# Optimization experiments

Hardware: AMD Instinct MI355X
Metric: run time of the kernel (lower is better)

## Reference

```python
import jax, jax.numpy as jnp
import numpy as np

B, L, D, H, R, E = 4, 2048, 256, 4, 128, 32768
HD = D // H  # head dim of long-range attention
FF = 4 * D   # positionwise FFN hidden
NEG_SLOPE = 0.2  # GATConv leaky_relu slope


def setup_inputs() -> dict:
    key = jax.random.key(0)
    ks = jax.random.split(key, 16)
    n = lambda k, sh: jax.random.normal(k, sh, dtype=jnp.float32) * 0.05
    z = lambda sh: jnp.zeros(sh, dtype=jnp.float32)
    o = lambda sh: jnp.ones(sh, dtype=jnp.float32)
    return {
        "s": jax.random.normal(ks[0], (B, L, D), dtype=jnp.float32),
        "gat_W": n(ks[1], (D, H * D)),
        "gat_att_src": n(ks[2], (H, D)),
        "gat_att_dst": n(ks[3], (H, D)),
        "gat_b": z((H * D,)),
        "short_W": n(ks[4], (H * D, D)), "short_b": z((D,)),
        "q_W": n(ks[5], (D, D)), "q_b": z((D,)),
        "k_W": n(ks[6], (D, D)), "k_b": z((D,)),
        "v_W": n(ks[7], (D, D)), "v_b": z((D,)),
        "o_W": n(ks[8], (D, D)), "o_b": z((D,)),
        "p_W": n(ks[9], (D, R)), "p_b": z((R,)),
        "lnq_g": o((D,)), "lnq_b": z((D,)),
        "lnk_g": o((D,)), "lnk_b": z((D,)),
        "lnv_g": o((D,)), "lnv_b": z((D,)),
        "ln1_g": o((D,)), "ln1_b": z((D,)),
        "ln2_g": o((D,)), "ln2_b": z((D,)),
        "f1_W": n(ks[10], (D, FF)), "f1_b": z((FF,)),
        "f2_W": n(ks[11], (FF, D)), "f2_b": z((D,)),
        "edge_index": jax.random.randint(ks[12], (2, E), 0, L, dtype=jnp.int32),
    }


def _ln(x, g, b, eps=1e-5):
    mu = jnp.mean(x, -1, keepdims=True)
    var = jnp.mean(jnp.square(x - mu), -1, keepdims=True)
    return (x - mu) * jax.lax.rsqrt(var + eps) * g + b


def _forward(p, edge_index):
    s = p["s"]
    loop = jnp.arange(L, dtype=edge_index.dtype)  # add_self_loops=True
    src = jnp.concatenate([edge_index[0], loop])
    dst = jnp.concatenate([edge_index[1], loop])

    def gat_one(x):  # x: [L, D] -> [L, H*D]  (PyG GATConv, concat=True)
        h = (x @ p["gat_W"]).reshape(L, H, D)
        a_src = jnp.einsum("nhc,hc->nh", h, p["gat_att_src"])
        a_dst = jnp.einsum("nhc,hc->nh", h, p["gat_att_dst"])
        e = jax.nn.leaky_relu(a_src[src] + a_dst[dst], NEG_SLOPE)  # [Etot, H]
        m = jax.ops.segment_max(e, dst, num_segments=L)            # scatter softmax
        ex = jnp.exp(e - m[dst])
        den = jax.ops.segment_sum(ex, dst, num_segments=L)
        alpha = ex / den[dst]
        out = jax.ops.segment_sum(h[src] * alpha[:, :, None], dst, num_segments=L)
        return out.reshape(L, H * D) + p["gat_b"]

    short = jax.vmap(gat_one)(s) @ p["short_W"] + p["short_b"]  # [B,L,D]

    # DynamicLongRange (Linformer-style dynamic projection)
    q = _ln(s @ p["q_W"] + p["q_b"], p["lnq_g"], p["lnq_b"])
    k = _ln(s @ p["k_W"] + p["k_b"], p["lnk_g"], p["lnk_b"])
    v = _ln(s @ p["v_W"] + p["v_b"], p["lnv_g"], p["lnv_b"])
    pm = jax.nn.softmax(k @ p["p_W"] + p["p_b"], axis=1)          # [B,L,R], softmax over seq
    k_c = jnp.einsum("blr,bld->brd", pm, k).reshape(B, R, H, HD)
    v_c = jnp.einsum("blr,bld->brd", pm, v).reshape(B, R, H, HD)
    q_h = q.reshape(B, L, H, HD)
    scores = jnp.einsum("blhd,brhd->bhlr", q_h, k_c) / jnp.sqrt(jnp.float32(HD))
    probs = jax.nn.softmax(scores, axis=-1)
    lng = jnp.einsum("bhlr,brhd->blhd", probs, v_c).reshape(B, L, D)
    lng = lng @ p["o_W"] + p["o_b"]

    # fuse short + long, residual + LN, then positionwise FFN + residual + LN
    h1 = _ln(s + short + lng, p["ln1_g"], p["ln1_b"])
    ff = jax.nn.relu(h1 @ p["f1_W"] + p["f1_b"]) @ p["f2_W"] + p["f2_b"]
    return _ln(h1 + ff, p["ln2_g"], p["ln2_b"])


def reference(s, gat_W, gat_att_src, gat_att_dst, gat_b, short_W, short_b,
              q_W, q_b, k_W, k_b, v_W, v_b, o_W, o_b, p_W, p_b,
              lnq_g, lnq_b, lnk_g, lnk_b, lnv_g, lnv_b,
              ln1_g, ln1_b, ln2_g, ln2_b, f1_W, f1_b, f2_W, f2_b, edge_index):
    p = dict(s=s, gat_W=gat_W, gat_att_src=gat_att_src, gat_att_dst=gat_att_dst,
             gat_b=gat_b, short_W=short_W, short_b=short_b, q_W=q_W, q_b=q_b,
             k_W=k_W, k_b=k_b, v_W=v_W, v_b=v_b, o_W=o_W, o_b=o_b, p_W=p_W,
             p_b=p_b, lnq_g=lnq_g, lnq_b=lnq_b, lnk_g=lnk_g, lnk_b=lnk_b,
             lnv_g=lnv_g, lnv_b=lnv_b, ln1_g=ln1_g, ln1_b=ln1_b, ln2_g=ln2_g,
             ln2_b=ln2_b, f1_W=f1_W, f1_b=f1_b, f2_W=f2_W, f2_b=f2_b)
    return _forward(p, edge_index)
```

## Files before the change

### kernel.cpp

```cpp
#include <hip/hip_runtime.h>
#include <math.h>

#define BB   4
#define LSEQ 2048
#define DV   256
#define HH   4
#define RR   128
#define EE   32768
#define ETOT (EE + LSEQ)
#define FFD  1024

typedef unsigned short u16;
typedef __attribute__((ext_vector_type(8))) short bf16x8;
typedef __attribute__((ext_vector_type(4))) float f32x4;

__device__ __forceinline__ u16 f2bf(float f) {
    union { float f; unsigned u; } x; x.f = f;
    unsigned r = x.u + 0x7fff + ((x.u >> 16) & 1);
    return (u16)(r >> 16);
}
__device__ __forceinline__ float bf2f(u16 u) {
    union { unsigned u; float f; } x; x.u = ((unsigned)u) << 16;
    return x.f;
}

__device__ __forceinline__ void gload16(const void* g, void* l) {
    __builtin_amdgcn_global_load_lds(
        (const __attribute__((address_space(1))) unsigned int*)g,
        (__attribute__((address_space(3))) unsigned int*)l, 16, 0, 0);
}

template<int BM, int BN, int OUTBF16, int ACT>
__global__ __launch_bounds__(256) void mfma_gemm_k(
    const u16* __restrict__ A, const u16* __restrict__ BT,
    const float* __restrict__ bias, void* __restrict__ Cv,
    int M, int N, int K, int lda, int ldb, int ldc,
    long bsA1, long bsA2, long bsB1, long bsB2, long bsC1, long bsC2,
    int subH, long pairB, long pairC, int ksl, int split, float alpha)
{
    constexpr int BK = 64;
    __shared__ u16 As[BM * BK];
    __shared__ u16 Bs[BN * BK];

    int z = blockIdx.z;
    int zb = z / subH, zh = z - zb * subH;
    int mtiles = M / BM;
    int pair = blockIdx.y / mtiles;
    int mt   = blockIdx.y - pair * mtiles;

    const u16* Ab = A  + zb * bsA1 + zh * bsA2;
    const u16* Bb = BT + zb * bsB1 + zh * bsB2 + (long)pair * pairB;
    int kstart = split ? zh * ksl : 0;
    int kcount = split ? ksl : K;
    int m0 = mt * BM, n0 = blockIdx.x * BN;

    int tid  = threadIdx.x;
    int wave = tid >> 6, lane = tid & 63;
    constexpr int WGN = (BN == 128) ? 2 : 1;
    constexpr int WGM = 4 / WGN;
    constexpr int MI  = BM / (WGM * 16);
    constexpr int NI  = BN / (WGN * 16);
    int wm = wave / WGN, wn = wave - wm * WGN;
    int wmo = wm * (MI * 16);
    int wno = wn * (NI * 16);

    f32x4 acc[MI][NI];
#pragma unroll
    for (int mi = 0; mi < MI; ++mi)
#pragma unroll
        for (int ni = 0; ni < NI; ++ni)
            acc[mi][ni] = (f32x4){0.f, 0.f, 0.f, 0.f};

    constexpr int AIT = (BM * BK / 8) / 256;
    constexpr int BIT = (BN * BK / 8) / 256;

    for (int k0 = 0; k0 < kcount; k0 += BK) {
        int kb = kstart + k0;
#pragma unroll
        for (int i = 0; i < AIT; ++i) {
            int p   = i * 256 + tid;
            int row = p >> 3;
            int kc  = (p & 7) ^ (row & 7);
            const u16* gp = Ab + (long)(m0 + row) * lda + kb + kc * 8;
            gload16(gp, (char*)As + (size_t)(i * 256 + wave * 64) * 16);
        }
#pragma unroll
        for (int i = 0; i < BIT; ++i) {
            int p   = i * 256 + tid;
            int row = p >> 3;
            int kc  = (p & 7) ^ (row & 7);
            const u16* gp = Bb + (long)(n0 + row) * ldb + kb + kc * 8;
            gload16(gp, (char*)Bs + (size_t)(i * 256 + wave * 64) * 16);
        }
        asm volatile("s_waitcnt vmcnt(0)");
        __syncthreads();

        const char* Ac = (const char*)As;
        const char* Bc = (const char*)Bs;
#pragma unroll
        for (int kh = 0; kh < 2; ++kh) {
            bf16x8 af[MI], bfr[NI];
            int kby = kh * 64 + ((lane >> 4) << 4);
#pragma unroll
            for (int mi = 0; mi < MI; ++mi) {
                int r = wmo + mi * 16 + (lane & 15);
                af[mi] = *(const bf16x8*)(Ac + r * 128 + (kby ^ ((r & 7) << 4)));
            }
#pragma unroll
            for (int ni = 0; ni < NI; ++ni) {
                int r = wno + ni * 16 + (lane & 15);
                bfr[ni] = *(const bf16x8*)(Bc + r * 128 + (kby ^ ((r & 7) << 4)));
            }
#pragma unroll
            for (int mi = 0; mi < MI; ++mi)
#pragma unroll
                for (int ni = 0; ni < NI; ++ni)
                    acc[mi][ni] = __builtin_amdgcn_mfma_f32_16x16x32_bf16(
                        af[mi], bfr[ni], acc[mi][ni], 0, 0, 0);
        }
        __syncthreads();
    }

    long cb = zb * bsC1 + zh * bsC2 + (long)pair * pairC;
#pragma unroll
    for (int mi = 0; mi < MI; ++mi) {
#pragma unroll
        for (int ni = 0; ni < NI; ++ni) {
            int col = n0 + wno + ni * 16 + (lane & 15);
            float bv = bias ? bias[col] : 0.f;
#pragma unroll
            for (int j = 0; j < 4; ++j) {
                int row = m0 + wmo + mi * 16 + ((lane >> 4) << 2) + j;
                float v = acc[mi][ni][j] * alpha + bv;
                if (ACT) v = fmaxf(v, 0.f);
                long idx = (long)row * ldc + col + cb;
                if (OUTBF16) ((u16*)Cv)[idx] = f2bf(v);
                else         ((float*)Cv)[idx] = v;
            }
        }
    }
}

template<int MODE, int BM>
__global__ __launch_bounds__(256) void gemm_ln_k(
    const u16* __restrict__ A, const u16* __restrict__ BT,
    const float* __restrict__ bias, int K, int lda,
    const float* __restrict__ lg0, const float* __restrict__ lb0,
    const float* __restrict__ lg1, const float* __restrict__ lb1,
    const float* __restrict__ lg2, const float* __restrict__ lb2,
    const u16* __restrict__ resB0, const u16* __restrict__ resB1,
    u16* __restrict__ outRM, u16* __restrict__ outRM2,
    u16* __restrict__ outT, float* __restrict__ outF)
{
    constexpr int BK = 64;
    constexpr int MI = BM / 16;
    constexpr int ABYTES = BM * 128;
    __shared__ char smem[ABYTES + 32768];
    __shared__ float redS[BM][4], redQ[BM][4];
    u16* Asm = (u16*)smem;
    u16* Bsm = (u16*)(smem + ABYTES);

    int seg = blockIdx.x;
    int m0 = blockIdx.y * BM;
    int n0 = seg * 256;
    int tid = threadIdx.x, wave = tid >> 6, lane = tid & 63;
    int c = lane & 15, g = lane >> 4;

    f32x4 acc[MI][4];
#pragma unroll
    for (int mi = 0; mi < MI; ++mi)
#pragma unroll
        for (int ni = 0; ni < 4; ++ni)
            acc[mi][ni] = (f32x4){0.f, 0.f, 0.f, 0.f};

    constexpr int AIT = (BM * BK / 8) / 256;

    for (int k0 = 0; k0 < K; k0 += BK) {
#pragma unroll
        for (int i = 0; i < AIT; ++i) {
            int p   = i * 256 + tid;
            int row = p >> 3;
            int kc  = (p & 7) ^ (row & 7);
            gload16(A + (long)(m0 + row) * lda + k0 + kc * 8,
                    smem + (size_t)(i * 256 + wave * 64) * 16);
        }
#pragma unroll
        for (int i = 0; i < 8; ++i) {
            int p   = i * 256 + tid;
            int row = p >> 3;
            int kc  = (p & 7) ^ (row & 7);
            gload16(BT + (long)(n0 + row) * K + k0 + kc * 8,
                    smem + ABYTES + (size_t)(i * 256 + wave * 64) * 16);
        }
        asm volatile("s_waitcnt vmcnt(0)");
        __syncthreads();

        const char* Ac = (const char*)Asm;
        const char* Bc = (const char*)Bsm;
#pragma unroll
        for (int kh = 0; kh < 2; ++kh) {
            bf16x8 af[MI], bfr[4];
            int kby = kh * 64 + (g << 4);
#pragma unroll
            for (int mi = 0; mi < MI; ++mi) {
                int r = mi * 16 + c;
                af[mi] = *(const bf16x8*)(Ac + r * 128 + (kby ^ ((r & 7) << 4)));
            }
#pragma unroll
            for (int ni = 0; ni < 4; ++ni) {
                int r = wave * 64 + ni * 16 + c;
                bfr[ni] = *(const bf16x8*)(Bc + r * 128 + (kby ^ ((r & 7) << 4)));
            }
#pragma unroll
            for (int mi = 0; mi < MI; ++mi)
#pragma unroll
                for (int ni = 0; ni < 4; ++ni)
                    acc[mi][ni] = __builtin_amdgcn_mfma_f32_16x16x32_bf16(
                        af[mi], bfr[ni], acc[mi][ni], 0, 0, 0);
        }
        __syncthreads();
    }

#pragma unroll
    for (int mi = 0; mi < MI; ++mi)
#pragma unroll
        for (int ni = 0; ni < 4; ++ni) {
            int colL = wave * 64 + ni * 16 + c;
            float bv = bias[n0 + colL];
#pragma unroll
            for (int j = 0; j < 4; ++j) {
                int row = mi * 16 + g * 4 + j;
                float v = acc[mi][ni][j] + bv;
                if (MODE == 1) {
                    long idx = (long)(m0 + row) * 256 + colL;
                    v += bf2f(resB0[idx]) + bf2f(resB1[idx]);
                }
                if (MODE == 2) {
                    long idx = (long)(m0 + row) * 256 + colL;
                    v += bf2f(resB0[idx]);
                }
                acc[mi][ni][j] = v;
            }
        }

#pragma unroll
    for (int mi = 0; mi < MI; ++mi)
#pragma unroll
        for (int j = 0; j < 4; ++j) {
            float s1 = 0.f, q1 = 0.f;
#pragma unroll
            for (int ni = 0; ni < 4; ++ni) {
                float v = acc[mi][ni][j];
                s1 += v; q1 += v * v;
            }
#pragma unroll
            for (int m = 1; m <= 8; m <<= 1) {
                s1 += __shfl_xor(s1, m);
                q1 += __shfl_xor(q1, m);
            }
            if (c == 0) {
                int row = mi * 16 + g * 4 + j;
                redS[row][wave] = s1;
                redQ[row][wave] = q1;
            }
        }
    __syncthreads();

    const float* gam;
    const float* bet;
    if (MODE == 0) {
        gam = (seg == 0) ? lg0 : (seg == 1) ? lg1 : lg2;
        bet = (seg == 0) ? lb0 : (seg == 1) ? lb1 : lb2;
    } else { gam = lg0; bet = lb0; }

    u16* T = (u16*)smem;

    float gv[4], bv2[4];
#pragma unroll
    for (int ni = 0; ni < 4; ++ni) {
        int colL = wave * 64 + ni * 16 + c;
        gv[ni] = gam[colL];
        bv2[ni] = bet[colL];
    }

#pragma unroll
    for (int mi = 0; mi < MI; ++mi)
#pragma unroll
        for (int j = 0; j < 4; ++j) {
            int row = mi * 16 + g * 4 + j;
            float S = redS[row][0] + redS[row][1] + redS[row][2] + redS[row][3];
            float Q = redQ[row][0] + redQ[row][1] + redQ[row][2] + redQ[row][3];
            float mu = S * (1.0f / 256.f);
            float var = Q * (1.0f / 256.f) - mu * mu;
            float rs = rsqrtf(var + 1e-5f);
#pragma unroll
            for (int ni = 0; ni < 4; ++ni) {
                int colL = wave * 64 + ni * 16 + c;
                float o = (acc[mi][ni][j] - mu) * rs * gv[ni] + bv2[ni];
                long idx = (long)(m0 + row) * 256 + colL;
                if (MODE == 0) {
                    u16 ob = f2bf(o);
                    if (seg == 0)      outRM[idx]  = ob;
                    else if (seg == 1) { outRM2[idx] = ob; T[colL * 65 + row] = ob; }
                    else               T[colL * 65 + row] = ob;
                } else if (MODE == 1) {
                    outRM[idx] = f2bf(o);
                } else {
                    outF[idx] = o;
                }
            }
        }

    if (MODE == 0 && seg >= 1) {
        __syncthreads();
        int b = m0 >> 11;
        int l0 = m0 & 2047;
        u16* dst = outT + ((seg == 2) ? 2097152 : 0)
                 + (long)b * 524288 + (long)tid * 2048 + l0;
        const u16* src = T + tid * 65;
#pragma unroll
        for (int i = 0; i < 8; ++i) {
            u16 tmp[8];
#pragma unroll
            for (int k2 = 0; k2 < 8; ++k2) tmp[k2] = src[i * 8 + k2];
            *(uint4*)(dst + i * 8) = *(uint4*)tmp;
        }
    }
}

__global__ __launch_bounds__(256) void attn_k(
    const u16* __restrict__ qb, const u16* __restrict__ kcb,
    const u16* __restrict__ vcT, u16* __restrict__ lngb)
{
    __shared__ u16 Ps[64 * 128];

    int bh = blockIdx.y;
    int b = bh >> 2, h = bh & 3;
    int l0 = blockIdx.x * 64;
    int tid = threadIdx.x, wave = tid >> 6, lane = tid & 63;
    int c = lane & 15, g = lane >> 4;

    const u16* kc = kcb + (long)b * (RR * DV) + h * 64;
    const u16* qg = qb + ((long)(b * LSEQ + l0)) * DV + h * 64;
    const u16* vg = vcT + ((long)b * DV + h * 64) * RR;

    f32x4 acc[8];
#pragma unroll
    for (int mi = 0; mi < 8; ++mi) acc[mi] = (f32x4){0.f, 0.f, 0.f, 0.f};

#pragma unroll
    for (int kh = 0; kh < 2; ++kh) {
        bf16x8 bq = *(const bf16x8*)(qg + (long)(wave * 16 + c) * DV + kh * 32 + g * 8);
#pragma unroll
        for (int mi = 0; mi < 8; ++mi) {
            bf16x8 af = *(const bf16x8*)(kc + (long)(mi * 16 + c) * DV + kh * 32 + g * 8);
            acc[mi] = __builtin_amdgcn_mfma_f32_16x16x32_bf16(af, bq, acc[mi], 0, 0, 0);
        }
    }

    float mx = -INFINITY;
#pragma unroll
    for (int mi = 0; mi < 8; ++mi)
#pragma unroll
        for (int j = 0; j < 4; ++j) {
            acc[mi][j] *= 0.125f;
            mx = fmaxf(mx, acc[mi][j]);
        }
    mx = fmaxf(mx, __shfl_xor(mx, 16));
    mx = fmaxf(mx, __shfl_xor(mx, 32));
    float den = 0.f;
#pragma unroll
    for (int mi = 0; mi < 8; ++mi)
#pragma unroll
        for (int j = 0; j < 4; ++j) {
            acc[mi][j] = __expf(acc[mi][j] - mx);
            den += acc[mi][j];
        }
    den += __shfl_xor(den, 16);
    den += __shfl_xor(den, 32);
    float inv = 1.0f / den;

    int l = wave * 16 + c;
#pragma unroll
    for (int mi = 0; mi < 8; ++mi) {
        short4 sv;
        sv.x = (short)f2bf(acc[mi][0] * inv);
        sv.y = (short)f2bf(acc[mi][1] * inv);
        sv.z = (short)f2bf(acc[mi][2] * inv);
        sv.w = (short)f2bf(acc[mi][3] * inv);
        int byte = l * 256 + ((mi * 32 + g * 8) ^ ((l & 7) << 4));
        *(short4*)((char*)Ps + byte) = sv;
    }
    __syncthreads();

    f32x4 a2[4];
#pragma unroll
    for (int ni = 0; ni < 4; ++ni) a2[ni] = (f32x4){0.f, 0.f, 0.f, 0.f};
#pragma unroll
    for (int kb = 0; kb < 4; ++kb) {
        int kby = kb * 64 + (g << 4);
        bf16x8 pa = *(const bf16x8*)((char*)Ps + l * 256 + (kby ^ ((l & 7) << 4)));
#pragma unroll
        for (int ni = 0; ni < 4; ++ni) {
            bf16x8 vf = *(const bf16x8*)(vg + (long)(ni * 16 + c) * RR + kb * 32 + g * 8);
            a2[ni] = __builtin_amdgcn_mfma_f32_16x16x32_bf16(pa, vf, a2[ni], 0, 0, 0);
        }
    }
#pragma unroll
    for (int ni = 0; ni < 4; ++ni)
#pragma unroll
        for (int j = 0; j < 4; ++j) {
            int lr = wave * 16 + g * 4 + j;
            int dh = ni * 16 + c;
            lngb[((long)(b * LSEQ + l0 + lr)) * DV + h * 64 + dh] = f2bf(a2[ni][j]);
        }
}

struct WTD { const float* src; u16* dst; int K, N, toff; };
struct WTA { WTD d[9]; };

__global__ __launch_bounds__(256) void prep_k(WTA a,
    const float* __restrict__ sin, u16* __restrict__ sout,
    const float* qb_, const float* kb_, const float* vb_,
    float* qkvb, int* icnt)
{
    int bid = blockIdx.x;
    if (bid < 1312) {
        int di = 0;
#pragma unroll
        for (int i = 1; i < 9; ++i) if (bid >= a.d[i].toff) di = i;
        const float* src = a.d[di].src;
        u16* dst = a.d[di].dst;
        int K = a.d[di].K, N = a.d[di].N;
        int tix = bid - a.d[di].toff;
        int nx = N >> 5;
        int tn = tix % nx, tk = tix / nx;
        int n0 = tn * 32, k0 = tk * 32;

        __shared__ float t[32][33];
        int tx = threadIdx.x & 31, ty = threadIdx.x >> 5;
#pragma unroll
        for (int i = 0; i < 32; i += 8)
            t[ty + i][tx] = src[(long)(k0 + ty + i) * N + n0 + tx];
        __syncthreads();
#pragma unroll
        for (int i = 0; i < 32; i += 8)
            dst[(long)(n0 + ty + i) * K + k0 + tx] = f2bf(t[tx][ty + i]);
    } else if (bid < 3360) {
        int i = ((bid - 1312) * 256 + threadIdx.x) * 4;
        float4 v = *(const float4*)(sin + i);
        sout[i]     = f2bf(v.x);
        sout[i + 1] = f2bf(v.y);
        sout[i + 2] = f2bf(v.z);
        sout[i + 3] = f2bf(v.w);
    } else if (bid == 3360) {
        int i = threadIdx.x;
#pragma unroll
        for (int rep = 0; rep < 3; ++rep) {
            int j = i + rep * 256;
            qkvb[j] = (j < 256) ? qb_[j] : ((j < 512) ? kb_[j - 256] : vb_[j - 512]);
        }
    } else {
        int t = (bid - 3361) * 256 + threadIdx.x;
        if (t < 512) ((int4*)icnt)[t] = (int4){0, 0, 0, 0};
    }
}

__global__ __launch_bounds__(256) void gat_att_k(
    const u16* __restrict__ h, const float* __restrict__ att_src,
    const float* __restrict__ att_dst, float* __restrict__ a_src,
    float* __restrict__ a_dst)
{
    int row  = blockIdx.x * 4 + (threadIdx.x >> 6);
    int lane = threadIdx.x & 63;
    int c0   = lane * 16;
    int head = lane >> 4;

    float as[16], ad[16];
#pragma unroll
    for (int i = 0; i < 16; ++i) { as[i] = att_src[c0 + i]; ad[i] = att_dst[c0 + i]; }

    const u16* hr = h + (long)row * (HH * DV) + c0;
    bf16x8 v0 = *(const bf16x8*)(hr);
    bf16x8 v1 = *(const bf16x8*)(hr + 8);
    float ps = 0.f, pd = 0.f;
#pragma unroll
    for (int i = 0; i < 8; ++i) {
        float f0 = bf2f((u16)v0[i]), f1 = bf2f((u16)v1[i]);
        ps += f0 * as[i] + f1 * as[i + 8];
        pd += f0 * ad[i] + f1 * ad[i + 8];
    }
#pragma unroll
    for (int m = 1; m <= 8; m <<= 1) {
        ps += __shfl_xor(ps, m);
        pd += __shfl_xor(pd, m);
    }
    if ((lane & 15) == 0) {
        a_src[(long)row * HH + head] = ps;
        a_dst[(long)row * HH + head] = pd;
    }
}

__global__ void csr_count_k(const int* __restrict__ ei, int* __restrict__ cnt)
{
    int i = blockIdx.x * blockDim.x + threadIdx.x;
    if (i >= ETOT) return;
    int dst = (i < EE) ? ei[EE + i] : (i - EE);
    atomicAdd(&cnt[dst], 1);
}

__global__ __launch_bounds__(256) void csr_scan_k(const int* __restrict__ cnt, int* __restrict__ off)
{
    __shared__ int chunk[256];
    int tid = threadIdx.x;
    int base = tid * 8;
    int loc[8];
    int s = 0;
#pragma unroll
    for (int i = 0; i < 8; ++i) { loc[i] = s; s += cnt[base + i]; }
    chunk[tid] = s;
    __syncthreads();
    for (int st = 1; st < 256; st <<= 1) {
        int v = (tid >= st) ? chunk[tid - st] : 0;
        __syncthreads();
        chunk[tid] += v;
        __syncthreads();
    }
    int pre = (tid == 0) ? 0 : chunk[tid - 1];
#pragma unroll
    for (int i = 0; i < 8; ++i) off[base + i] = pre + loc[i];
    if (tid == 255) off[LSEQ] = chunk[255];
}

__global__ void csr_fill_k(const int* __restrict__ ei, const int* __restrict__ off,
                           int* __restrict__ cnt, int* __restrict__ bucket)
{
    int i = blockIdx.x * blockDim.x + threadIdx.x;
    if (i >= ETOT) return;
    int dst = (i < EE) ? ei[EE + i] : (i - EE);
    int p = atomicSub(&cnt[dst], 1) - 1;
    bucket[off[dst] + p] = i;
}

__global__ __launch_bounds__(256) void gat_gather_k(
    const u16* __restrict__ h, const int* __restrict__ ei,
    const int* __restrict__ off, const int* __restrict__ bucket,
    const float* __restrict__ a_src, const float* __restrict__ a_dst,
    const float* __restrict__ gat_b, u16* __restrict__ out)
{
    int wv = threadIdx.x >> 6, lane = threadIdx.x & 63;
    int id = blockIdx.x;
    int jg = id >> 3, r8 = id & 7;
    int b  = r8 >> 1;
    int n  = (jg * 2 + (r8 & 1)) * 4 + wv;
    int beg = off[n], deg = off[n + 1] - beg;

    __shared__ int   src_sh[4][64];
    __shared__ float ex_sh[4][64][4];

    const float* asrc_b = a_src + (long)b * LSEQ * HH;
    const float4 ad4 = *(const float4*)(a_dst + ((long)b * LSEQ + n) * HH);
    float adst[4] = { ad4.x, ad4.y, ad4.z, ad4.w };

    int hd = lane >> 4;
    const u16* hb = h + (long)b * LSEQ * (HH * DV) + lane * 16;
    float acc[16];
#pragma unroll
    for (int i = 0; i < 16; ++i) acc[i] = 0.f;
    float sm[4] = { 0.f, 0.f, 0.f, 0.f };

    for (int c0 = 0; c0 < deg; c0 += 64) {
        int idx = c0 + lane;
        if (idx < deg) {
            int eid = bucket[beg + idx];
            int src = (eid < EE) ? ei[eid] : (eid - EE);
            src_sh[wv][lane] = src;
            float4 as4 = *(const float4*)(asrc_b + (long)src * HH);
            float as[4] = { as4.x, as4.y, as4.z, as4.w };
#pragma unroll
            for (int hh = 0; hh < 4; ++hh) {
                float e = as[hh] + adst[hh];
                e = (e >= 0.f) ? e : 0.2f * e;
                float ex = __expf(e);
                ex_sh[wv][lane][hh] = ex;
                sm[hh] += ex;
            }
        }
        int cn = deg - c0; if (cn > 64) cn = 64;
#pragma unroll 2
        for (int j = 0; j < cn; ++j) {
            int src = src_sh[wv][j];
            float al = ex_sh[wv][j][hd];
            const u16* p = hb + (long)src * (HH * DV);
            bf16x8 v0 = *(const bf16x8*)p;
            bf16x8 v1 = *(const bf16x8*)(p + 8);
#pragma unroll
            for (int i = 0; i < 8; ++i) {
                acc[i]     += al * bf2f((u16)v0[i]);
                acc[i + 8] += al * bf2f((u16)v1[i]);
            }
        }
    }

#pragma unroll
    for (int hh = 0; hh < 4; ++hh)
#pragma unroll
        for (int m = 32; m >= 1; m >>= 1)
            sm[hh] += __shfl_xor(sm[hh], m);
    float inv = 1.0f / sm[hd];

    u16 o16[16];
    const float* gb = gat_b + lane * 16;
#pragma unroll
    for (int i = 0; i < 16; ++i) o16[i] = f2bf(acc[i] * inv + gb[i]);
    uint4* op = (uint4*)(out + ((long)b * LSEQ + n) * (HH * DV) + lane * 16);
    op[0] = ((uint4*)o16)[0];
    op[1] = ((uint4*)o16)[1];
}

__global__ __launch_bounds__(256) void colsoftmax_k(const float* __restrict__ pm,
                                                    u16* __restrict__ pmT)
{
    int r = blockIdx.x;
    int b = blockIdx.y;
    int tid = threadIdx.x, wave = tid >> 6, lane = tid & 63;
    const float* base = pm + (long)b * LSEQ * RR + r;
    u16* obase = pmT + ((long)b * RR + r) * LSEQ;

    float x[8];
#pragma unroll
    for (int i = 0; i < 8; ++i) x[i] = base[(long)(tid + i * 256) * RR];

    __shared__ float red[4];
    __shared__ float m_sh, d_sh;
    float mx = x[0];
#pragma unroll
    for (int i = 1; i < 8; ++i) mx = fmaxf(mx, x[i]);
#pragma unroll
    for (int m = 32; m >= 1; m >>= 1) mx = fmaxf(mx, __shfl_xor(mx, m));
    if (lane == 0) red[wave] = mx;
    __syncthreads();
    if (tid == 0) m_sh = fmaxf(fmaxf(red[0], red[1]), fmaxf(red[2], red[3]));
    __syncthreads();
    float m = m_sh;
    float sm = 0.f;
#pragma unroll
    for (int i = 0; i < 8; ++i) { x[i] = __expf(x[i] - m); sm += x[i]; }
#pragma unroll
    for (int mm = 32; mm >= 1; mm >>= 1) sm += __shfl_xor(sm, mm);
    if (lane == 0) red[wave] = sm;
    __syncthreads();
    if (tid == 0) d_sh = red[0] + red[1] + red[2] + red[3];
    __syncthreads();
    float inv = 1.0f / d_sh;
#pragma unroll
    for (int i = 0; i < 8; ++i) obase[tid + i * 256] = f2bf(x[i] * inv);
}

__global__ __launch_bounds__(256) void reduce_kvc_k(
    const float* __restrict__ part, u16* __restrict__ kvcb, u16* __restrict__ vcT)
{
    int pb = blockIdx.z;
    int pair = pb >> 2, b = pb & 3;
    int r0 = blockIdx.y * 32, d0 = blockIdx.x * 64;
    int tid = threadIdx.x;
    __shared__ float t[32][65];
    const float* pp = part + (long)pb * (16 * 32768);
    int r = tid >> 6;
    int d = tid & 63;
#pragma unroll
    for (int i = 0; i < 8; ++i) {
        int rr = r0 + r + i * 4;
        float s = 0.f;
#pragma unroll
        for (int sp = 0; sp < 16; ++sp)
            s += pp[(long)sp * 32768 + rr * 256 + d0 + d];
        kvcb[(long)pb * 32768 + rr * 256 + d0 + d] = f2bf(s);
        t[r + i * 4][d] = s;
    }
    if (pair == 0) return;
    __syncthreads();
    int dd = tid >> 2, rb = (tid & 3) * 8;
    u16 o8[8];
#pragma unroll
    for (int k = 0; k < 8; ++k) o8[k] = f2bf(t[rb + k][dd]);
    *(uint4*)(vcT + ((long)(b * 256 + d0 + dd)) * 128 + r0 + rb) = *(uint4*)o8;
}

extern "C" void kernel_launch(void* const* d_in, const int* in_sizes, int n_in,
                              void* d_out, int out_size, void* d_ws, size_t ws_size,
                              hipStream_t stream)
{
    const float* s        = (const float*)d_in[0];
    const float* gat_W    = (const float*)d_in[1];
    const float* att_src  = (const float*)d_in[2];
    const float* att_dst  = (const float*)d_in[3];
    const float* gat_b    = (const float*)d_in[4];
    const float* short_W  = (const float*)d_in[5];
    const float* short_b  = (const float*)d_in[6];
    const float* q_W      = (const float*)d_in[7];
    const float* q_b      = (const float*)d_in[8];
    const float* k_W      = (const float*)d_in[9];
    const float* k_b      = (const float*)d_in[10];
    const float* v_W      = (const float*)d_in[11];
    const float* v_b      = (const float*)d_in[12];
    const float* o_W      = (const float*)d_in[13];
    const float* o_b      = (const float*)d_in[14];
    const float* p_W      = (const float*)d_in[15];
    const float* p_b      = (const float*)d_in[16];
    const float* lnq_g    = (const float*)d_in[17];
    const float* lnq_b    = (const float*)d_in[18];
    const float* lnk_g    = (const float*)d_in[19];
    const float* lnk_b    = (const float*)d_in[20];
    const float* lnv_g    = (const float*)d_in[21];
    const float* lnv_b    = (const float*)d_in[22];
    const float* ln1_g    = (const float*)d_in[23];
    const float* ln1_b    = (const float*)d_in[24];
    const float* ln2_g    = (const float*)d_in[25];
    const float* ln2_b    = (const float*)d_in[26];
    const float* f1_W     = (const float*)d_in[27];
    const float* f1_b     = (const float*)d_in[28];
    const float* f2_W     = (const float*)d_in[29];
    const float* f2_b     = (const float*)d_in[30];
    const int*   ei       = (const int*)d_in[31];
    float* out = (float*)d_out;

    const size_t MB = 1024 * 1024;
    char* W = (char*)d_ws;
    u16*   sb      = (u16*)(W);
    u16*   gatT    = (u16*)(W + 4*MB);
    u16*   shortT  = (u16*)(W + 4*MB + 524288);
    u16*   qkvT    = (u16*)(W + 4*MB + 1048576);
    u16*   oT      = (u16*)(W + 4*MB + 1441792);
    u16*   pT      = (u16*)(W + 4*MB + 1572864);
    u16*   f1T     = (u16*)(W + 4*MB + 1638400);
    u16*   f2T     = (u16*)(W + 4*MB + 2162688);
    float* qkvb    = (float*)(W + 4*MB + 2686976);
    int*   ioff    = (int*)(W + 4*MB + 2690048);
    int*   icnt    = (int*)(W + 4*MB + 2699264);
    int*   ibucket = (int*)(W + 4*MB + 2707456);
    u16*   h       = (u16*)(W + 8*MB);
    u16*   ffh     = (u16*)(W + 8*MB);
    u16*   gat_out = (u16*)(W + 24*MB);
    u16*   h1b     = (u16*)(W + 40*MB);
    u16*   shortb16= (u16*)(W + 44*MB);
    float* pmraw   = (float*)(W + 48*MB);
    float* part    = (float*)(W + 48*MB);
    u16*   lngb    = (u16*)(W + 48*MB);
    u16*   qb      = (u16*)(W + 72*MB);
    u16*   kb      = (u16*)(W + 76*MB);
    u16*   kvT     = (u16*)(W + 84*MB);
    u16*   pmT     = (u16*)(W + 92*MB);
    u16*   kvcb    = (u16*)(W + 94*MB);
    u16*   vcT     = (u16*)(W + 94*MB + 524288);
    float* a_src   = (float*)(W + 95*MB);
    float* a_dst   = (float*)(W + 95*MB + 131072);

    const int ML = BB * LSEQ;

    WTA wa;
    wa.d[0] = { gat_W,   gatT,            256, 1024, 0    };
    wa.d[1] = { short_W, shortT,         1024,  256, 256  };
    wa.d[2] = { q_W,     qkvT,            256,  256, 512  };
    wa.d[3] = { k_W,     qkvT + 65536,    256,  256, 576  };
    wa.d[4] = { v_W,     qkvT + 131072,   256,  256, 640  };
    wa.d[5] = { o_W,     oT,              256,  256, 704  };
    wa.d[6] = { p_W,     pT,              256,  128, 768  };
    wa.d[7] = { f1_W,    f1T,             256, 1024, 800  };
    wa.d[8] = { f2_W,    f2T,            1024,  256, 1056 };
    prep_k<<<3363, 256, 0, stream>>>(wa, s, sb, q_b, k_b, v_b, qkvb, icnt);

    csr_count_k<<<(ETOT + 255) / 256, 256, 0, stream>>>(ei, icnt);
    csr_scan_k<<<1, 256, 0, stream>>>(icnt, ioff);
    csr_fill_k<<<(ETOT + 255) / 256, 256, 0, stream>>>(ei, ioff, icnt, ibucket);

    mfma_gemm_k<128, 128, 1, 0><<<dim3(8, 64, 1), 256, 0, stream>>>(
        sb, gatT, nullptr, h, ML, 1024, 256, 256, 256, 1024,
        0, 0, 0, 0, 0, 0, 1, 0, 0, 0, 0, 1.f);
    gat_att_k<<<ML / 4, 256, 0, stream>>>(h, att_src, att_dst, a_src, a_dst);
    gat_gather_k<<<2048, 256, 0, stream>>>(h, ei, ioff, ibucket,
                                           a_src, a_dst, gat_b, gat_out);
    mfma_gemm_k<64, 128, 1, 0><<<dim3(2, 128, 1), 256, 0, stream>>>(
        gat_out, shortT, short_b, shortb16, ML, 256, 1024, 1024, 1024, 256,
        0, 0, 0, 0, 0, 0, 1, 0, 0, 0, 0, 1.f);

    gemm_ln_k<0, 64><<<dim3(3, 128), 256, 0, stream>>>(
        sb, qkvT, qkvb, 256, 256,
        lnq_g, lnq_b, lnk_g, lnk_b, lnv_g, lnv_b,
        nullptr, nullptr, qb, kb, kvT, nullptr);

    mfma_gemm_k<64, 64, 0, 0><<<dim3(2, 128, 1), 256, 0, stream>>>(
        kb, pT, p_b, pmraw, ML, 128, 256, 256, 256, 128,
        0, 0, 0, 0, 0, 0, 1, 0, 0, 0, 0, 1.f);
    colsoftmax_k<<<dim3(RR, BB), 256, 0, stream>>>(pmraw, pmT);

    mfma_gemm_k<128, 128, 0, 0><<<dim3(2, 2, 64), 256, 0, stream>>>(
        pmT, kvT, nullptr, part, 128, 256, 2048, 2048, 2048, 256,
        262144, 0, 524288, 0, 524288, 32768, 16, 2097152, 2097152, 128, 1, 1.f);
    reduce_kvc_k<<<dim3(4, 4, 8), 256, 0, stream>>>(part, kvcb, vcT);

    attn_k<<<dim3(LSEQ / 64, BB * HH), 256, 0, stream>>>(qb, kvcb, vcT, lngb);

    gemm_ln_k<1, 32><<<dim3(1, 256), 256, 0, stream>>>(
        lngb, oT, o_b, 256, 256,
        ln1_g, ln1_b, nullptr, nullptr, nullptr, nullptr,
        sb, shortb16, h1b, nullptr, nullptr, nullptr);

    mfma_gemm_k<128, 128, 1, 1><<<dim3(8, 64, 1), 256, 0, stream>>>(
        h1b, f1T, f1_b, ffh, ML, 1024, 256, 256, 256, 1024,
        0, 0, 0, 0, 0, 0, 1, 0, 0, 0, 0, 1.f);

    gemm_ln_k<2, 32><<<dim3(1, 256), 256, 0, stream>>>(
        ffh, f2T, f2_b, 1024, 1024,
        ln2_g, ln2_b, nullptr, nullptr, nullptr, nullptr,
        h1b, nullptr, nullptr, nullptr, nullptr, out);
}
```

Before: 195.4 us.

## Fuse short projection GEMM into o-proj LN kernel and build CSR in one block

The short-range projection GEMM (gat_out @ short_W) becomes a second accumulation pass inside the o-projection+LN1 kernel, so its bf16 intermediate is never written to or read back from global memory. The CSR build (count, scan, fill) is collapsed into one single-block kernel that uses shared-memory atomics, which removes three launches and the count-zeroing in prep. The cost is that the fused LN kernel now runs with only 256 blocks of BM=32 over K=1024+256, which may underuse the GPU. The single-block CSR build also serialises about 35K edges on one CU.

```diff
diff --git a/kernel.cpp b/kernel.cpp
--- a/kernel.cpp
+++ b/kernel.cpp
@@ -145,16 +145,19 @@
 __global__ __launch_bounds__(256) void gemm_ln_k(
     const u16* __restrict__ A, const u16* __restrict__ BT,
     const float* __restrict__ bias, int K, int lda,
+    const u16* __restrict__ A2, const u16* __restrict__ BT2,
+    const float* __restrict__ bias2, int K2,
     const float* __restrict__ lg0, const float* __restrict__ lb0,
     const float* __restrict__ lg1, const float* __restrict__ lb1,
     const float* __restrict__ lg2, const float* __restrict__ lb2,
-    const u16* __restrict__ resB0, const u16* __restrict__ resB1,
+    const u16* __restrict__ resB0,
     u16* __restrict__ outRM, u16* __restrict__ outRM2,
     u16* __restrict__ outT, float* __restrict__ outF)
 {
     constexpr int BK = 64;
     constexpr int MI = BM / 16;
     constexpr int ABYTES = BM * 128;
+    constexpr int NPASS = (MODE == 1) ? 2 : 1;
     __shared__ char smem[ABYTES + 32768];
     __shared__ float redS[BM][4], redQ[BM][4];
     u16* Asm = (u16*)smem;
@@ -175,50 +178,58 @@
 
     constexpr int AIT = (BM * BK / 8) / 256;
 
-    for (int k0 = 0; k0 < K; k0 += BK) {
-#pragma unroll
-        for (int i = 0; i < AIT; ++i) {
-            int p   = i * 256 + tid;
-            int row = p >> 3;
-            int kc  = (p & 7) ^ (row & 7);
-            gload16(A + (long)(m0 + row) * lda + k0 + kc * 8,
-                    smem + (size_t)(i * 256 + wave * 64) * 16);
-        }
-#pragma unroll
-        for (int i = 0; i < 8; ++i) {
-            int p   = i * 256 + tid;
-            int row = p >> 3;
-            int kc  = (p & 7) ^ (row & 7);
-            gload16(BT + (long)(n0 + row) * K + k0 + kc * 8,
-                    smem + ABYTES + (size_t)(i * 256 + wave * 64) * 16);
-        }
-        asm volatile("s_waitcnt vmcnt(0)");
-        __syncthreads();
-
-        const char* Ac = (const char*)Asm;
-        const char* Bc = (const char*)Bsm;
-#pragma unroll
-        for (int kh = 0; kh < 2; ++kh) {
-            bf16x8 af[MI], bfr[4];
-            int kby = kh * 64 + (g << 4);
-#pragma unroll
-            for (int mi = 0; mi < MI; ++mi) {
-                int r = mi * 16 + c;
-                af[mi] = *(const bf16x8*)(Ac + r * 128 + (kby ^ ((r & 7) << 4)));
-            }
-#pragma unroll
-            for (int ni = 0; ni < 4; ++ni) {
-                int r = wave * 64 + ni * 16 + c;
-                bfr[ni] = *(const bf16x8*)(Bc + r * 128 + (kby ^ ((r & 7) << 4)));
-            }
-#pragma unroll
-            for (int mi = 0; mi < MI; ++mi)
-#pragma unroll
-                for (int ni = 0; ni < 4; ++ni)
-                    acc[mi][ni] = __builtin_amdgcn_mfma_f32_16x16x32_bf16(
-                        af[mi], bfr[ni], acc[mi][ni], 0, 0, 0);
-        }
-        __syncthreads();
+#pragma unroll 1
+    for (int pass = 0; pass < NPASS; ++pass) {
+        const u16* Ap  = (pass == 0) ? A  : A2;
+        const u16* Bp  = (pass == 0) ? BT : BT2;
+        int Kp   = (pass == 0) ? K : K2;
+        int ldap = (pass == 0) ? lda : K2;
+
+        for (int k0 = 0; k0 < Kp; k0 += BK) {
+#pragma unroll
+            for (int i = 0; i < AIT; ++i) {
+                int p   = i * 256 + tid;
+                int row = p >> 3;
+                int kc  = (p & 7) ^ (row & 7);
+                gload16(Ap + (long)(m0 + row) * ldap + k0 + kc * 8,
+                        smem + (size_t)(i * 256 + wave * 64) * 16);
+            }
+#pragma unroll
+            for (int i = 0; i < 8; ++i) {
+                int p   = i * 256 + tid;
+                int row = p >> 3;
+                int kc  = (p & 7) ^ (row & 7);
+                gload16(Bp + (long)(n0 + row) * Kp + k0 + kc * 8,
+                        smem + ABYTES + (size_t)(i * 256 + wave * 64) * 16);
+            }
+            asm volatile("s_waitcnt vmcnt(0)");
+            __syncthreads();
+
+            const char* Ac = (const char*)Asm;
+            const char* Bc = (const char*)Bsm;
+#pragma unroll
+            for (int kh = 0; kh < 2; ++kh) {
+                bf16x8 af[MI], bfr[4];
+                int kby = kh * 64 + (g << 4);
+#pragma unroll
+                for (int mi = 0; mi < MI; ++mi) {
+                    int r = mi * 16 + c;
+                    af[mi] = *(const bf16x8*)(Ac + r * 128 + (kby ^ ((r & 7) << 4)));
+                }
+#pragma unroll
+                for (int ni = 0; ni < 4; ++ni) {
+                    int r = wave * 64 + ni * 16 + c;
+                    bfr[ni] = *(const bf16x8*)(Bc + r * 128 + (kby ^ ((r & 7) << 4)));
+                }
+#pragma unroll
+                for (int mi = 0; mi < MI; ++mi)
+#pragma unroll
+                    for (int ni = 0; ni < 4; ++ni)
+                        acc[mi][ni] = __builtin_amdgcn_mfma_f32_16x16x32_bf16(
+                            af[mi], bfr[ni], acc[mi][ni], 0, 0, 0);
+            }
+            __syncthreads();
+        }
     }
 
 #pragma unroll
@@ -227,15 +238,12 @@
         for (int ni = 0; ni < 4; ++ni) {
             int colL = wave * 64 + ni * 16 + c;
             float bv = bias[n0 + colL];
+            if (MODE == 1) bv += bias2[colL];
 #pragma unroll
             for (int j = 0; j < 4; ++j) {
                 int row = mi * 16 + g * 4 + j;
                 float v = acc[mi][ni][j] + bv;
-                if (MODE == 1) {
-                    long idx = (long)(m0 + row) * 256 + colL;
-                    v += bf2f(resB0[idx]) + bf2f(resB1[idx]);
-                }
-                if (MODE == 2) {
+                if (MODE == 1 || MODE == 2) {
                     long idx = (long)(m0 + row) * 256 + colL;
                     v += bf2f(resB0[idx]);
                 }
@@ -422,7 +430,7 @@
 __global__ __launch_bounds__(256) void prep_k(WTA a,
     const float* __restrict__ sin, u16* __restrict__ sout,
     const float* qb_, const float* kb_, const float* vb_,
-    float* qkvb, int* icnt)
+    float* qkvb)
 {
     int bid = blockIdx.x;
     if (bid < 1312) {
@@ -453,16 +461,13 @@
         sout[i + 1] = f2bf(v.y);
         sout[i + 2] = f2bf(v.z);
         sout[i + 3] = f2bf(v.w);
-    } else if (bid == 3360) {
+    } else {
         int i = threadIdx.x;
 #pragma unroll
         for (int rep = 0; rep < 3; ++rep) {
             int j = i + rep * 256;
             qkvb[j] = (j < 256) ? qb_[j] : ((j < 512) ? kb_[j - 256] : vb_[j - 512]);
         }
-    } else {
-        int t = (bid - 3361) * 256 + threadIdx.x;
-        if (t < 512) ((int4*)icnt)[t] = (int4){0, 0, 0, 0};
     }
 }
 
@@ -501,45 +506,41 @@
     }
 }
 
-__global__ void csr_count_k(const int* __restrict__ ei, int* __restrict__ cnt)
-{
-    int i = blockIdx.x * blockDim.x + threadIdx.x;
-    if (i >= ETOT) return;
-    int dst = (i < EE) ? ei[EE + i] : (i - EE);
-    atomicAdd(&cnt[dst], 1);
-}
-
-__global__ __launch_bounds__(256) void csr_scan_k(const int* __restrict__ cnt, int* __restrict__ off)
-{
-    __shared__ int chunk[256];
+__global__ __launch_bounds__(1024) void csr_build_k(
+    const int* __restrict__ ei, int* __restrict__ off, int* __restrict__ bucket)
+{
+    __shared__ int cnt[2048];
+    __shared__ int wsum[1024];
     int tid = threadIdx.x;
-    int base = tid * 8;
-    int loc[8];
-    int s = 0;
-#pragma unroll
-    for (int i = 0; i < 8; ++i) { loc[i] = s; s += cnt[base + i]; }
-    chunk[tid] = s;
-    __syncthreads();
-    for (int st = 1; st < 256; st <<= 1) {
-        int v = (tid >= st) ? chunk[tid - st] : 0;
+    cnt[tid] = 0; cnt[tid + 1024] = 0;
+    __syncthreads();
+    for (int i = tid; i < ETOT; i += 1024) {
+        int dst = (i < EE) ? ei[EE + i] : (i - EE);
+        atomicAdd(&cnt[dst], 1);
+    }
+    __syncthreads();
+    int a = cnt[tid * 2], b = cnt[tid * 2 + 1];
+    wsum[tid] = a + b;
+    __syncthreads();
+    for (int st = 1; st < 1024; st <<= 1) {
+        int v = (tid >= st) ? wsum[tid - st] : 0;
         __syncthreads();
-        chunk[tid] += v;
+        wsum[tid] += v;
         __syncthreads();
     }
-    int pre = (tid == 0) ? 0 : chunk[tid - 1];
-#pragma unroll
-    for (int i = 0; i < 8; ++i) off[base + i] = pre + loc[i];
-    if (tid == 255) off[LSEQ] = chunk[255];
-}
-
-__global__ void csr_fill_k(const int* __restrict__ ei, const int* __restrict__ off,
-                           int* __restrict__ cnt, int* __restrict__ bucket)
-{
-    int i = blockIdx.x * blockDim.x + threadIdx.x;
-    if (i >= ETOT) return;
-    int dst = (i < EE) ? ei[EE + i] : (i - EE);
-    int p = atomicSub(&cnt[dst], 1) - 1;
-    bucket[off[dst] + p] = i;
+    int pre = (tid == 0) ? 0 : wsum[tid - 1];
+    off[tid * 2]     = pre;
+    off[tid * 2 + 1] = pre + a;
+    if (tid == 1023) off[2048] = wsum[1023];
+    __syncthreads();
+    cnt[tid * 2]     = pre;
+    cnt[tid * 2 + 1] = pre + a;
+    __syncthreads();
+    for (int i = tid; i < ETOT; i += 1024) {
+        int dst = (i < EE) ? ei[EE + i] : (i - EE);
+        int p = atomicAdd(&cnt[dst], 1);
+        bucket[p] = i;
+    }
 }
 
 __global__ __launch_bounds__(256) void gat_gather_k(
@@ -737,13 +738,11 @@
     u16*   f2T     = (u16*)(W + 4*MB + 2162688);
     float* qkvb    = (float*)(W + 4*MB + 2686976);
     int*   ioff    = (int*)(W + 4*MB + 2690048);
-    int*   icnt    = (int*)(W + 4*MB + 2699264);
     int*   ibucket = (int*)(W + 4*MB + 2707456);
     u16*   h       = (u16*)(W + 8*MB);
     u16*   ffh     = (u16*)(W + 8*MB);
     u16*   gat_out = (u16*)(W + 24*MB);
     u16*   h1b     = (u16*)(W + 40*MB);
-    u16*   shortb16= (u16*)(W + 44*MB);
     float* pmraw   = (float*)(W + 48*MB);
     float* part    = (float*)(W + 48*MB);
     u16*   lngb    = (u16*)(W + 48*MB);
@@ -768,11 +767,9 @@
     wa.d[6] = { p_W,     pT,              256,  128, 768  };
     wa.d[7] = { f1_W,    f1T,             256, 1024, 800  };
     wa.d[8] = { f2_W,    f2T,            1024,  256, 1056 };
-    prep_k<<<3363, 256, 0, stream>>>(wa, s, sb, q_b, k_b, v_b, qkvb, icnt);
-
-    csr_count_k<<<(ETOT + 255) / 256, 256, 0, stream>>>(ei, icnt);
-    csr_scan_k<<<1, 256, 0, stream>>>(icnt, ioff);
-    csr_fill_k<<<(ETOT + 255) / 256, 256, 0, stream>>>(ei, ioff, icnt, ibucket);
+    prep_k<<<3361, 256, 0, stream>>>(wa, s, sb, q_b, k_b, v_b, qkvb);
+
+    csr_build_k<<<1, 1024, 0, stream>>>(ei, ioff, ibucket);
 
     mfma_gemm_k<128, 128, 1, 0><<<dim3(8, 64, 1), 256, 0, stream>>>(
         sb, gatT, nullptr, h, ML, 1024, 256, 256, 256, 1024,
@@ -780,14 +777,12 @@
     gat_att_k<<<ML / 4, 256, 0, stream>>>(h, att_src, att_dst, a_src, a_dst);
     gat_gather_k<<<2048, 256, 0, stream>>>(h, ei, ioff, ibucket,
                                            a_src, a_dst, gat_b, gat_out);
-    mfma_gemm_k<64, 128, 1, 0><<<dim3(2, 128, 1), 256, 0, stream>>>(
-        gat_out, shortT, short_b, shortb16, ML, 256, 1024, 1024, 1024, 256,
-        0, 0, 0, 0, 0, 0, 1, 0, 0, 0, 0, 1.f);
 
     gemm_ln_k<0, 64><<<dim3(3, 128), 256, 0, stream>>>(
         sb, qkvT, qkvb, 256, 256,
+        nullptr, nullptr, nullptr, 0,
         lnq_g, lnq_b, lnk_g, lnk_b, lnv_g, lnv_b,
-        nullptr, nullptr, qb, kb, kvT, nullptr);
+        nullptr, qb, kb, kvT, nullptr);
 
     mfma_gemm_k<64, 64, 0, 0><<<dim3(2, 128, 1), 256, 0, stream>>>(
         kb, pT, p_b, pmraw, ML, 128, 256, 256, 256, 128,
@@ -803,8 +798,9 @@
 
     gemm_ln_k<1, 32><<<dim3(1, 256), 256, 0, stream>>>(
         lngb, oT, o_b, 256, 256,
+        gat_out, shortT, short_b, 1024,
         ln1_g, ln1_b, nullptr, nullptr, nullptr, nullptr,
-        sb, shortb16, h1b, nullptr, nullptr, nullptr);
+        sb, h1b, nullptr, nullptr, nullptr);
 
     mfma_gemm_k<128, 128, 1, 1><<<dim3(8, 64, 1), 256, 0, stream>>>(
         h1b, f1T, f1_b, ffh, ML, 1024, 256, 256, 256, 1024,
@@ -812,6 +808,7 @@
 
     gemm_ln_k<2, 32><<<dim3(1, 256), 256, 0, stream>>>(
         ffh, f2T, f2_b, 1024, 1024,
+        nullptr, nullptr, nullptr, 0,
         ln2_g, ln2_b, nullptr, nullptr, nullptr, nullptr,
-        h1b, nullptr, nullptr, nullptr, nullptr, out);
-}
+        h1b, nullptr, nullptr, nullptr, out);
+}
```

Result: slower. 208.3 us (+6.6%).
